# Kernel optimization log

Hardware: AMD Instinct MI355X
Metric: run time of the kernel (lower is better)

The kernel has to match this reference:

```python
import jax, jax.numpy as jnp
import numpy as np

N_HEAD = 16
QMIN, QMAX = 0.0, 255.0  # 8-bit asymmetric


def fake_quantize(x, scale, zp):
    # LearnableFakeQuantize (asymmetric, 8-bit) with straight-through round.
    q = x / scale + zp
    q = q + jax.lax.stop_gradient(jnp.round(q) - q)  # STE round
    q = jnp.clip(q, QMIN, QMAX)
    return (q - zp) * scale


def setup_inputs() -> dict:
    key = jax.random.key(0)
    ks = jax.random.split(key, 4)
    B, T, C = 2, 2048, 1024
    return {
        "hidden_states": jax.random.normal(ks[0], (B, T, C), jnp.float32),
        "W_attn": jax.random.normal(ks[1], (C, 3 * C), jnp.float32) * (1.0 / np.sqrt(C)),
        "b_attn": jnp.zeros((3 * C,), jnp.float32),
        "W_proj": jax.random.normal(ks[2], (C, C), jnp.float32) * (1.0 / np.sqrt(C)),
        "b_proj": jnp.zeros((C,), jnp.float32),
        "kv_scale": jnp.full((1,), 0.05, jnp.float32),
        "kv_zp": jnp.full((1,), 128.0, jnp.float32),
    }


def reference(hidden_states, W_attn, b_attn, W_proj, b_proj, kv_scale, kv_zp):
    B, T, C = hidden_states.shape
    H = N_HEAD
    D = C // H
    qkv = hidden_states @ W_attn + b_attn            # [B,T,3C]
    q, k, v = jnp.split(qkv, 3, axis=2)
    # [B,T,C] -> [B,H,T,D]
    q = q.reshape(B, T, H, D).transpose(0, 2, 1, 3)
    k = k.reshape(B, T, H, D).transpose(0, 2, 1, 3)
    v = v.reshape(B, T, H, D).transpose(0, 2, 1, 3)
    k = fake_quantize(k, kv_scale, kv_zp)
    v = fake_quantize(v, kv_scale, kv_zp)
    scores = jnp.einsum("bhqd,bhkd->bhqk", q, k) / jnp.sqrt(jnp.asarray(D, q.dtype))
    causal = jnp.tril(jnp.ones((T, T), bool))        # bias[:T,:T]
    scores = jnp.where(causal, scores, jnp.asarray(-jnp.inf, scores.dtype))
    attn = jax.nn.softmax(scores, axis=-1)
    out = jnp.einsum("bhqk,bhkd->bhqd", attn, v)     # [B,H,T,D]
    out = out.transpose(0, 2, 1, 3).reshape(B, T, C)
    return out @ W_proj + b_proj
```

## Files before the change

kernel.cpp:

```cpp
#include <hip/hip_runtime.h>
#include <math.h>

#define TB 2048
#define CC 1024
#define NH 16
#define HD 64

typedef __bf16 bf16x8 __attribute__((ext_vector_type(8)));
typedef __bf16 bf16x4 __attribute__((ext_vector_type(4)));
typedef float  f32x4  __attribute__((ext_vector_type(4)));

__device__ inline float exp2fast(float x) { return __builtin_amdgcn_exp2f(x); }

__device__ __forceinline__ void gl_lds16(const __bf16* g, __bf16* l) {
    __builtin_amdgcn_global_load_lds(
        (const __attribute__((address_space(1))) void*)g,
        (__attribute__((address_space(3))) void*)l, 16, 0, 0);
}

__global__ __launch_bounds__(256)
void cvt_kernel(const float* __restrict__ src, __bf16* __restrict__ dst) {
    int i = (blockIdx.x * 256 + threadIdx.x) * 4;
    f32x4 v = *(const f32x4*)&src[i];
    bf16x4 o;
    o.x = (__bf16)v.x; o.y = (__bf16)v.y; o.z = (__bf16)v.z; o.w = (__bf16)v.w;
    *(bf16x4*)&dst[i] = o;
}

__global__ __launch_bounds__(256)
void tpose_kernel(const float* __restrict__ src, __bf16* __restrict__ dst,
                  int K, int N) {
    __shared__ __bf16 L[64][68];
    const int tid = threadIdx.x;
    const int n0 = blockIdx.x * 64, k0 = blockIdx.y * 64;
    #pragma unroll
    for (int i = 0; i < 4; i++) {
        int id = tid + i * 256;
        int r = id >> 4, c = (id & 15) * 4;
        f32x4 v = *(const f32x4*)&src[(size_t)(k0 + r) * N + n0 + c];
        bf16x4 o;
        o.x = (__bf16)v.x; o.y = (__bf16)v.y; o.z = (__bf16)v.z; o.w = (__bf16)v.w;
        *(bf16x4*)&L[r][c] = o;
    }
    __syncthreads();
    #pragma unroll
    for (int i = 0; i < 4; i++) {
        int id = tid + i * 256;
        int nr = id >> 4, kc = (id & 15) * 4;
        bf16x4 o;
        o.x = L[kc + 0][nr]; o.y = L[kc + 1][nr];
        o.z = L[kc + 2][nr]; o.w = L[kc + 3][nr];
        *(bf16x4*)&dst[(size_t)(n0 + nr) * K + k0 + kc] = o;
    }
}

template<int BN, int MODE>
__global__ __launch_bounds__(256)
void gemm_bt(const __bf16* __restrict__ A, const __bf16* __restrict__ Bt,
             const float* __restrict__ bias,
             __bf16* __restrict__ o0, __bf16* __restrict__ o1,
             __bf16* __restrict__ o2, float* __restrict__ of,
             int M, int N, int K,
             const float* __restrict__ scp, const float* __restrict__ zpp)
{
    constexpr int NT = BN / 32;
    __shared__ __bf16 Asm[128][32];
    __shared__ __bf16 Bsm[BN][32];

    const int tid  = threadIdx.x;
    const int m0   = blockIdx.y * 128;
    const int n0   = blockIdx.x * BN;
    const int w    = tid >> 6, lane = tid & 63;
    const int wm   = (w & 1) * 64, wn = (w >> 1) * (BN / 2);
    const int r16  = lane & 15, quad = lane >> 4;
    const int srow = lane >> 2, scol = (lane & 3) * 8;

    f32x4 acc[4][NT];
    #pragma unroll
    for (int i = 0; i < 4; i++)
        #pragma unroll
        for (int j = 0; j < NT; j++) acc[i][j] = 0.f;

    for (int k0 = 0; k0 < K; k0 += 32) {
        #pragma unroll
        for (int p = 0; p < 2; p++)
            gl_lds16(&A[(size_t)(m0 + p * 64 + w * 16 + srow) * K + k0 + scol],
                     &Asm[p * 64 + w * 16][0]);
        #pragma unroll
        for (int p = 0; p < BN / 64; p++)
            gl_lds16(&Bt[(size_t)(n0 + p * 64 + w * 16 + srow) * K + k0 + scol],
                     &Bsm[p * 64 + w * 16][0]);
        __syncthreads();

        bf16x8 af[4], bfr[NT];
        #pragma unroll
        for (int mt = 0; mt < 4; mt++)
            af[mt] = *(const bf16x8*)&Asm[wm + mt * 16 + r16][quad * 8];
        #pragma unroll
        for (int nt = 0; nt < NT; nt++)
            bfr[nt] = *(const bf16x8*)&Bsm[wn + nt * 16 + r16][quad * 8];
        #pragma unroll
        for (int mt = 0; mt < 4; mt++)
            #pragma unroll
            for (int nt = 0; nt < NT; nt++)
                acc[mt][nt] = __builtin_amdgcn_mfma_f32_16x16x32_bf16(
                    af[mt], bfr[nt], acc[mt][nt], 0, 0, 0);
        __syncthreads();
    }

    const float sc = scp[0];
    const float zp = zpp[0];

    #pragma unroll
    for (int mt = 0; mt < 4; mt++) {
        #pragma unroll
        for (int nt = 0; nt < NT; nt++) {
            #pragma unroll
            for (int r = 0; r < 4; r++) {
                int gm = m0 + wm + mt * 16 + quad * 4 + r;
                int gn = n0 + wn + nt * 16 + r16;
                float val = acc[mt][nt][r] + bias[gn];
                if (MODE == 1) {
                    of[(size_t)gm * N + gn] = val;
                } else {
                    int part = gn >> 10;
                    int idx  = gn & 1023;
                    int h = idx >> 6, d = idx & 63;
                    int b = gm >> 11, t = gm & 2047;
                    size_t off = (((size_t)(b * NH + h)) * TB + t) * HD + d;
                    if (part == 0) {
                        o0[off] = (__bf16)(val * 0.18033688f);
                    } else {
                        float qv = val / sc + zp;
                        qv = rintf(qv);
                        qv = fminf(fmaxf(qv, 0.f), 255.f);
                        float dq = (qv - zp) * sc;
                        if (part == 1) o1[off] = (__bf16)dq;
                        else           o2[off] = (__bf16)dq;
                    }
                }
            }
        }
    }
}

__global__ __launch_bounds__(256, 4)
void attn_mfma(const __bf16* __restrict__ Q, const __bf16* __restrict__ Kg,
               const __bf16* __restrict__ Vg, __bf16* __restrict__ O)
{
    __shared__ alignas(16) __bf16 Ksm[64][72];
    __shared__ alignas(16) __bf16 Vsm[64][72];

    const int tid  = threadIdx.x;
    const int qt   = 31 - (blockIdx.x >> 5);
    const int bh   = blockIdx.x & 31;
    const int q0   = qt * 64;
    const int w    = tid >> 6, lane = tid & 63;
    const int l15  = lane & 15, quad = lane >> 4;
    const int b    = bh >> 4, h = bh & 15;

    const int krow = tid >> 3;
    const int kseg = (tid & 7) * 8;
    const int vkey = tid & 63;
    const int vc   = tid >> 6;

    const __bf16* Kbh = Kg + (size_t)bh * TB * HD;
    const __bf16* Vbh = Vg + (size_t)bh * TB * HD;

    const __bf16* Qrow = Q + ((size_t)bh * TB + q0 + w * 16 + l15) * HD;
    bf16x8 qf0 = *(const bf16x8*)&Qrow[quad * 8];
    bf16x8 qf1 = *(const bf16x8*)&Qrow[32 + quad * 8];

    const int rbase = (l15 >> 2) * 8 + (l15 & 3);

    bf16x8 af_l;
    {
        __bf16 v = (l15 == 0) ? (__bf16)1.0f : (__bf16)0.0f;
        #pragma unroll
        for (int j = 0; j < 8; j++) af_l[j] = v;
    }

    f32x4 acc_o[4], acc_l;
    #pragma unroll
    for (int nt = 0; nt < 4; nt++) acc_o[nt] = 0.f;
    acc_l = 0.f;
    float mrun = -3.0e38f;

    bf16x8 kpre0 = *(const bf16x8*)&Kbh[(size_t)krow * HD + kseg];
    bf16x8 kpre1 = *(const bf16x8*)&Kbh[(size_t)(32 + krow) * HD + kseg];
    bf16x8 vpre0 = *(const bf16x8*)&Vbh[(size_t)vkey * HD + vc * 8];
    bf16x8 vpre1 = *(const bf16x8*)&Vbh[(size_t)vkey * HD + (4 + vc) * 8];

    for (int kt = 0; kt <= qt; kt++) {
        __syncthreads();
        *(bf16x8*)&Ksm[krow][kseg]      = kpre0;
        *(bf16x8*)&Ksm[32 + krow][kseg] = kpre1;
        #pragma unroll
        for (int j = 0; j < 8; j++) {
            Vsm[vc * 8 + j][vkey]      = vpre0[j];
            Vsm[32 + vc * 8 + j][vkey] = vpre1[j];
        }
        __syncthreads();

        if (kt < qt) {
            const __bf16* Kn = Kbh + (size_t)(kt + 1) * 64 * HD;
            const __bf16* Vn = Vbh + (size_t)(kt + 1) * 64 * HD;
            kpre0 = *(const bf16x8*)&Kn[(size_t)krow * HD + kseg];
            kpre1 = *(const bf16x8*)&Kn[(size_t)(32 + krow) * HD + kseg];
            vpre0 = *(const bf16x8*)&Vn[(size_t)vkey * HD + vc * 8];
            vpre1 = *(const bf16x8*)&Vn[(size_t)vkey * HD + (4 + vc) * 8];
        }

        const bool diag = (kt == qt);

        f32x4 s[4];
        #pragma unroll
        for (int nt = 0; nt < 4; nt++) s[nt] = 0.f;
        #pragma unroll
        for (int nt = 0; nt < 4; nt++) {
            if (diag && (nt & 1) && w < 2) continue;
            int row = rbase + (nt & 1) * 32 + ((nt >> 1) << 2);
            bf16x8 kf0 = *(const bf16x8*)&Ksm[row][quad * 8];
            bf16x8 kf1 = *(const bf16x8*)&Ksm[row][32 + quad * 8];
            s[nt] = __builtin_amdgcn_mfma_f32_16x16x32_bf16(kf0, qf0, s[nt], 0, 0, 0);
            s[nt] = __builtin_amdgcn_mfma_f32_16x16x32_bf16(kf1, qf1, s[nt], 0, 0, 0);
        }

        if (diag) {
            #pragma unroll
            for (int nt = 0; nt < 4; nt++) {
                int koff = (nt & 1) * 32 + ((nt >> 1) << 2) + quad * 8;
                #pragma unroll
                for (int r = 0; r < 4; r++)
                    if (koff + r > w * 16 + l15) s[nt][r] = -3.0e38f;
            }
        }

        float mx = s[0][0];
        #pragma unroll
        for (int nt = 0; nt < 4; nt++)
            #pragma unroll
            for (int r = 0; r < 4; r++) mx = fmaxf(mx, s[nt][r]);
        mx = fmaxf(mx, __shfl_xor(mx, 16));
        mx = fmaxf(mx, __shfl_xor(mx, 32));

        float mnew  = fmaxf(mrun, mx);
        float alpha = exp2fast(mrun - mnew);
        mrun = mnew;
        #pragma unroll
        for (int nt = 0; nt < 4; nt++)
            #pragma unroll
            for (int r = 0; r < 4; r++) acc_o[nt][r] *= alpha;
        acc_l[0] *= alpha;

        float p[4][4];
        #pragma unroll
        for (int nt = 0; nt < 4; nt++)
            #pragma unroll
            for (int r = 0; r < 4; r++) p[nt][r] = exp2fast(s[nt][r] - mnew);

        bf16x8 pf0, pf1;
        #pragma unroll
        for (int j = 0; j < 4; j++) {
            pf0[j]     = (__bf16)p[0][j];
            pf0[4 + j] = (__bf16)p[2][j];
            pf1[j]     = (__bf16)p[1][j];
            pf1[4 + j] = (__bf16)p[3][j];
        }

        acc_l = __builtin_amdgcn_mfma_f32_16x16x32_bf16(af_l, pf0, acc_l, 0, 0, 0);
        acc_l = __builtin_amdgcn_mfma_f32_16x16x32_bf16(af_l, pf1, acc_l, 0, 0, 0);

        #pragma unroll
        for (int nt = 0; nt < 4; nt++) {
            bf16x8 vf0 = *(const bf16x8*)&Vsm[nt * 16 + l15][quad * 8];
            bf16x8 vf1 = *(const bf16x8*)&Vsm[nt * 16 + l15][32 + quad * 8];
            acc_o[nt] = __builtin_amdgcn_mfma_f32_16x16x32_bf16(vf0, pf0, acc_o[nt], 0, 0, 0);
            acc_o[nt] = __builtin_amdgcn_mfma_f32_16x16x32_bf16(vf1, pf1, acc_o[nt], 0, 0, 0);
        }
    }

    float lall = __shfl(acc_l[0], l15);
    float inv  = 1.f / lall;
    size_t trow = (size_t)(b * TB) + q0 + w * 16 + l15;
    #pragma unroll
    for (int nt = 0; nt < 4; nt++) {
        bf16x4 st;
        #pragma unroll
        for (int r = 0; r < 4; r++) st[r] = (__bf16)(acc_o[nt][r] * inv);
        *(bf16x4*)&O[trow * CC + h * HD + nt * 16 + quad * 4] = st;
    }
}

extern "C" void kernel_launch(void* const* d_in, const int* in_sizes, int n_in,
                              void* d_out, int out_size, void* d_ws, size_t ws_size,
                              hipStream_t stream) {
    (void)in_sizes; (void)n_in; (void)out_size; (void)ws_size;
    const float* hidden   = (const float*)d_in[0];
    const float* W_attn   = (const float*)d_in[1];
    const float* b_attn   = (const float*)d_in[2];
    const float* W_proj   = (const float*)d_in[3];
    const float* b_proj   = (const float*)d_in[4];
    const float* kv_scale = (const float*)d_in[5];
    const float* kv_zp    = (const float*)d_in[6];
    float* out = (float*)d_out;

    __bf16* hb  = (__bf16*)d_ws;
    __bf16* wat = hb  + (size_t)4096 * 1024;
    __bf16* wpt = wat + (size_t)3072 * 1024;
    __bf16* qws = wpt + (size_t)1024 * 1024;
    __bf16* kws = qws + (size_t)2 * NH * TB * HD;
    __bf16* vws = kws + (size_t)2 * NH * TB * HD;
    __bf16* ows = vws + (size_t)2 * NH * TB * HD;

    cvt_kernel<<<4096, 256, 0, stream>>>(hidden, hb);
    tpose_kernel<<<dim3(48, 16), 256, 0, stream>>>(W_attn, wat, 1024, 3072);
    tpose_kernel<<<dim3(16, 16), 256, 0, stream>>>(W_proj, wpt, 1024, 1024);

    gemm_bt<128, 0><<<dim3(24, 32), 256, 0, stream>>>(
        hb, wat, b_attn, qws, kws, vws, nullptr, 4096, 3072, 1024, kv_scale, kv_zp);

    attn_mfma<<<dim3(32 * 32), 256, 0, stream>>>(qws, kws, vws, ows);

    gemm_bt<64, 1><<<dim3(16, 32), 256, 0, stream>>>(
        ows, wpt, b_proj, nullptr, nullptr, nullptr, out, 4096, 1024, 1024,
        kv_scale, kv_zp);
}
```

Measured before the change: 191.2 us.

## Swizzle GEMM LDS tiles and transpose MFMA operands for vectorized epilogue stores

The GEMM now XOR-swizzles the 16-byte column chunks in the A and B shared-memory tiles, on both the global-to-LDS load and the fragment read, to reduce LDS bank conflicts. It also swaps the MFMA operand order so each lane's accumulator holds four consecutive N columns. That lets the epilogue add bias and write output as 4-wide vector stores (f32x4 or bf16x4) instead of scalar strided stores. The risk is that the swizzle must match exactly between writer and reader, and the vector stores assume 16-byte and 8-byte alignment of the outputs.

```diff
diff --git a/kernel.cpp b/kernel.cpp
--- a/kernel.cpp
+++ b/kernel.cpp
@@ -73,13 +73,17 @@
     const int w    = tid >> 6, lane = tid & 63;
     const int wm   = (w & 1) * 64, wn = (w >> 1) * (BN / 2);
     const int r16  = lane & 15, quad = lane >> 4;
-    const int srow = lane >> 2, scol = (lane & 3) * 8;
-
-    f32x4 acc[4][NT];
-    #pragma unroll
-    for (int i = 0; i < 4; i++)
-        #pragma unroll
-        for (int j = 0; j < NT; j++) acc[i][j] = 0.f;
+    const int srow = lane >> 2;
+    const int ssw  = (srow + (srow >> 2)) & 3;
+    const int scol = ((lane & 3) ^ ssw) * 8;
+    const int rsw  = (r16 + (r16 >> 2)) & 3;
+    const int rcol = (quad ^ rsw) * 8;
+
+    f32x4 acc[NT][4];
+    #pragma unroll
+    for (int i = 0; i < NT; i++)
+        #pragma unroll
+        for (int j = 0; j < 4; j++) acc[i][j] = 0.f;
 
     for (int k0 = 0; k0 < K; k0 += 32) {
         #pragma unroll
@@ -95,16 +99,16 @@
         bf16x8 af[4], bfr[NT];
         #pragma unroll
         for (int mt = 0; mt < 4; mt++)
-            af[mt] = *(const bf16x8*)&Asm[wm + mt * 16 + r16][quad * 8];
+            af[mt] = *(const bf16x8*)&Asm[wm + mt * 16 + r16][rcol];
         #pragma unroll
         for (int nt = 0; nt < NT; nt++)
-            bfr[nt] = *(const bf16x8*)&Bsm[wn + nt * 16 + r16][quad * 8];
-        #pragma unroll
-        for (int mt = 0; mt < 4; mt++)
-            #pragma unroll
-            for (int nt = 0; nt < NT; nt++)
-                acc[mt][nt] = __builtin_amdgcn_mfma_f32_16x16x32_bf16(
-                    af[mt], bfr[nt], acc[mt][nt], 0, 0, 0);
+            bfr[nt] = *(const bf16x8*)&Bsm[wn + nt * 16 + r16][rcol];
+        #pragma unroll
+        for (int nt = 0; nt < NT; nt++)
+            #pragma unroll
+            for (int mt = 0; mt < 4; mt++)
+                acc[nt][mt] = __builtin_amdgcn_mfma_f32_16x16x32_bf16(
+                    bfr[nt], af[mt], acc[nt][mt], 0, 0, 0);
         __syncthreads();
     }
 
@@ -112,32 +116,36 @@
     const float zp = zpp[0];
 
     #pragma unroll
-    for (int mt = 0; mt < 4; mt++) {
-        #pragma unroll
-        for (int nt = 0; nt < NT; nt++) {
-            #pragma unroll
-            for (int r = 0; r < 4; r++) {
-                int gm = m0 + wm + mt * 16 + quad * 4 + r;
-                int gn = n0 + wn + nt * 16 + r16;
-                float val = acc[mt][nt][r] + bias[gn];
-                if (MODE == 1) {
-                    of[(size_t)gm * N + gn] = val;
+    for (int nt = 0; nt < NT; nt++) {
+        #pragma unroll
+        for (int mt = 0; mt < 4; mt++) {
+            int gm = m0 + wm + mt * 16 + r16;
+            int gn = n0 + wn + nt * 16 + quad * 4;
+            f32x4 val = acc[nt][mt] + *(const f32x4*)&bias[gn];
+            if (MODE == 1) {
+                *(f32x4*)&of[(size_t)gm * N + gn] = val;
+            } else {
+                int part = gn >> 10;
+                int idx  = gn & 1023;
+                int h = idx >> 6, d = idx & 63;
+                int b = gm >> 11, t = gm & 2047;
+                size_t off = (((size_t)(b * NH + h)) * TB + t) * HD + d;
+                bf16x4 st;
+                if (part == 0) {
+                    #pragma unroll
+                    for (int r = 0; r < 4; r++)
+                        st[r] = (__bf16)(val[r] * 0.18033688f);
+                    *(bf16x4*)&o0[off] = st;
                 } else {
-                    int part = gn >> 10;
-                    int idx  = gn & 1023;
-                    int h = idx >> 6, d = idx & 63;
-                    int b = gm >> 11, t = gm & 2047;
-                    size_t off = (((size_t)(b * NH + h)) * TB + t) * HD + d;
-                    if (part == 0) {
-                        o0[off] = (__bf16)(val * 0.18033688f);
-                    } else {
-                        float qv = val / sc + zp;
+                    #pragma unroll
+                    for (int r = 0; r < 4; r++) {
+                        float qv = val[r] / sc + zp;
                         qv = rintf(qv);
                         qv = fminf(fmaxf(qv, 0.f), 255.f);
-                        float dq = (qv - zp) * sc;
-                        if (part == 1) o1[off] = (__bf16)dq;
-                        else           o2[off] = (__bf16)dq;
+                        st[r] = (__bf16)((qv - zp) * sc);
                     }
+                    if (part == 1) *(bf16x4*)&o1[off] = st;
+                    else           *(bf16x4*)&o2[off] = st;
                 }
             }
         }
```

After: 194.0 us. About the same (+1.4%).
